# Optimization experiments

Hardware: AMD Instinct MI355X
Metric: run time of the kernel (lower is better)

Reference implementation:

```python
import jax, jax.numpy as jnp
import numpy as np

B, N, H = 8, 256, 128
IN_DIM = 2 * H + 3  # concat of row emb, col emb, 3-d edge embedding


def setup_inputs() -> dict:
    key = jax.random.key(0)
    ks = jax.random.split(key, 12)
    # xavier_uniform bound = sqrt(6/(fan_in+fan_out))
    def xavier(k, out_d, in_d, gain=1.0):
        bound = gain * np.sqrt(6.0 / (in_d + out_d))
        return jax.random.uniform(k, (out_d, in_d), jnp.float32, -bound, bound)
    return {
        "x_emb": jax.random.normal(ks[0], (B, N, H), jnp.float32),
        "pair_emb": jax.random.normal(ks[1], (B, N, N, H), jnp.float32),
        "pos": jax.random.normal(ks[2], (B, N, 3), jnp.float32),
        "coord_diff": jax.random.normal(ks[3], (B, N, N, 3), jnp.float32),
        "node_mask": jnp.ones((B, N, 1), jnp.float32),
        "pair_mask": jnp.ones((B, N, N, 1), jnp.float32),
        # dist_decoder: Linear(H, 3)
        "Wd": xavier(ks[4], 3, H),
        "bd": jnp.zeros((3,), jnp.float32),
        # coord_mlp: Linear(2H+3, H) -> SiLU -> Linear(H, H) -> SiLU -> Linear(H, 1, bias=False, gain=0.001)
        "W1": xavier(ks[5], H, IN_DIM),
        "b1": jnp.zeros((H,), jnp.float32),
        "W2": xavier(ks[6], H, H),
        "b2": jnp.zeros((H,), jnp.float32),
        "W3": xavier(ks[7], 1, H, gain=0.001),
    }


def reference(x_emb, pair_emb, pos, coord_diff, node_mask, pair_mask,
              Wd, bd, W1, b1, W2, b2, W3):
    # edge_emb: [B,N,N,3]
    edge_emb = jnp.einsum("bijh,dh->bijd", pair_emb, Wd) + bd
    # row/col broadcasts of node embeddings to pairwise shape [B,N,N,H]
    row = jnp.broadcast_to(x_emb[:, :, None, :], (B, N, N, H))
    col = jnp.broadcast_to(x_emb[:, None, :, :], (B, N, N, H))
    inp = jnp.concatenate([row, col, edge_emb], axis=-1)  # [B,N,N,2H+3]
    h = jax.nn.silu(jnp.einsum("bijk,hk->bijh", inp, W1) + b1)
    h = jax.nn.silu(jnp.einsum("bijh,gh->bijg", h, W2) + b2)
    s = jnp.einsum("bijh,oh->bijo", h, W3)  # [B,N,N,1]  (tanh=False path)
    trans = coord_diff * s * pair_mask  # [B,N,N,3]
    return pos + trans.sum(axis=2)
```

## Files before the change

kernel.cpp:

```cpp
#include <hip/hip_runtime.h>
#include <cstdint>
#include <cstddef>

#define B_ 8
#define N_ 256
#define H_ 128

typedef float f32x4 __attribute__((ext_vector_type(4)));
typedef int i32x4 __attribute__((ext_vector_type(4)));
typedef int i32x2 __attribute__((ext_vector_type(2)));
typedef __bf16 bf16x8 __attribute__((ext_vector_type(8)));
typedef unsigned int u32;
typedef unsigned short u16;

__device__ __forceinline__ u32 pack_bf16_pair(float lo, float hi) {
  u16 a = __builtin_bit_cast(u16, (__bf16)lo);
  u16 b = __builtin_bit_cast(u16, (__bf16)hi);
  return (u32)a | ((u32)b << 16);
}

__device__ __forceinline__ float silu_f(float x) {
  return x * __builtin_amdgcn_rcpf(1.0f + __expf(-x));
}

__device__ __forceinline__ f32x4 mfma16(i32x4 a, i32x4 b, f32x4 c) {
  return __builtin_amdgcn_mfma_f32_16x16x32_bf16(
      __builtin_bit_cast(bf16x8, a), __builtin_bit_cast(bf16x8, b), c, 0, 0, 0);
}

__global__ void prep_ru_kernel(const float* __restrict__ x_emb,
                               const float* __restrict__ W1,
                               const float* __restrict__ b1,
                               const float* __restrict__ bd,
                               float* __restrict__ R,
                               float* __restrict__ U) {
  __shared__ float xs[16][H_];
  const int t = threadIdx.x;
  const int row0 = blockIdx.x * 16;
#pragma unroll
  for (int r = 0; r < 16; ++r)
    xs[r][t] = x_emb[(size_t)(row0 + r) * H_ + t];
  __syncthreads();

  const float* w1g = W1 + (size_t)t * 259;
  float accR[16], accU[16];
#pragma unroll
  for (int r = 0; r < 16; ++r) { accR[r] = 0.f; accU[r] = 0.f; }
  for (int h = 0; h < H_; ++h) {
    float wa = w1g[h];
    float wb = w1g[128 + h];
#pragma unroll
    for (int r = 0; r < 16; ++r) {
      accR[r] += xs[r][h] * wa;
      accU[r] += xs[r][h] * wb;
    }
  }
  float bias = b1[t] + bd[0] * w1g[256] + bd[1] * w1g[257] + bd[2] * w1g[258];
#pragma unroll
  for (int r = 0; r < 16; ++r) {
    int n = (row0 + r) & (N_ - 1);
    R[(size_t)(row0 + r) * H_ + t] = accR[r];
    U[(size_t)(row0 + r) * H_ + (t ^ ((n & 7) << 2))] = accU[r] + bias;
  }
}

__global__ void prep_w_kernel(const float* __restrict__ W1,
                              const float* __restrict__ Wd,
                              const float* __restrict__ W2,
                              u16* __restrict__ We_b,
                              u16* __restrict__ W2_b) {
  const int idx = blockIdx.x * 256 + threadIdx.x;
  const int g = idx >> 7, h = idx & 127;
  const float* w1g = W1 + (size_t)g * 259 + 256;
  float we = w1g[0] * Wd[h] + w1g[1] * Wd[128 + h] + w1g[2] * Wd[256 + h];
  int se = (h >> 3) ^ (g & 7);
  We_b[g * 128 + (se << 3) + (h & 7)] = __builtin_bit_cast(u16, (__bf16)we);
  int s2 = (h >> 2) ^ (g & 7);
  W2_b[g * 128 + (s2 << 2) + (h & 3)] = __builtin_bit_cast(u16, (__bf16)W2[idx]);
}

__launch_bounds__(1024, 4)
__global__ void posupd_main(const float* __restrict__ pe,
                            const float* __restrict__ cd,
                            const float* __restrict__ pmask,
                            const float* __restrict__ b2,
                            const float* __restrict__ W3,
                            const float* __restrict__ R,
                            const float* __restrict__ U,
                            const uint4* __restrict__ Wcomb,
                            float* __restrict__ partial) {
  __shared__ uint4 ldsv[6144];
  char* lds = (char*)ldsv;
  const int tid = threadIdx.x;
  const int lane = tid & 63, wv = tid >> 6;
  const int bid = blockIdx.x;
  const int b = bid >> 8;
  const int rem = bid & 255;
  const int ig = rem >> 2, jg = rem & 3;

  const uint4* Usrc = (const uint4*)(U + ((size_t)b * N_ + jg * 64) * H_);
#pragma unroll
  for (int c = 0; c < 6; ++c) {
    int k = wv * 6 + c;
    const uint4* src = (k < 64) ? (Wcomb + (k << 6) + lane)
                                : (Usrc + ((k - 64) << 6) + lane);
    *reinterpret_cast<uint4*>(lds + (k << 10) + (lane << 4)) = *src;
  }
  __syncthreads();

  const int tok = lane & 15, kg = lane >> 4;
  const int iw = wv & 3, jtw = wv >> 2;
  const int i = ig * 4 + iw;
  const int jl = jtw * 16 + tok;
  const size_t bi = (size_t)b * N_ + i;
  const int jgl = jg * 64 + jl;

  const float* perow = pe + (bi * N_ + jgl) * H_;
  i32x4 bpe[4];
#pragma unroll
  for (int kt = 0; kt < 4; ++kt) {
    const float* p = perow + kt * 32 + kg * 8;
    f32x4 lo = *reinterpret_cast<const f32x4*>(p);
    f32x4 hi = *reinterpret_cast<const f32x4*>(p + 4);
    i32x4 f;
    f.x = (int)pack_bf16_pair(lo.x, lo.y);
    f.y = (int)pack_bf16_pair(lo.z, lo.w);
    f.z = (int)pack_bf16_pair(hi.x, hi.y);
    f.w = (int)pack_bf16_pair(hi.z, hi.w);
    bpe[kt] = f;
  }

  f32x4 a1[8];
#pragma unroll
  for (int mt = 0; mt < 8; ++mt) { a1[mt].x = a1[mt].y = a1[mt].z = a1[mt].w = 0.f; }
#pragma unroll
  for (int kt = 0; kt < 4; ++kt) {
#pragma unroll
    for (int mt = 0; mt < 8; ++mt) {
      int g = mt * 16 + tok;
      int off = (g << 8) + (((kt << 6) + (kg << 4)) ^ ((g & 7) << 4));
      i32x4 afr = *reinterpret_cast<const i32x4*>(lds + off);
      a1[mt] = mfma16(afr, bpe[kt], a1[mt]);
    }
  }

  const float* Rrow = R + bi * H_;
  u32 pk0[8], pk1[8];
#pragma unroll
  for (int mt = 0; mt < 8; ++mt) {
    int ch = mt * 16 + kg * 4;
    f32x4 rr = *reinterpret_cast<const f32x4*>(Rrow + ch);
    int ub = 65536 + (jl << 9) + ((ch << 2) ^ ((jl & 7) << 4));
    f32x4 uu = *reinterpret_cast<const f32x4*>(lds + ub);
    float h0 = silu_f(a1[mt].x + rr.x + uu.x);
    float h1 = silu_f(a1[mt].y + rr.y + uu.y);
    float h2 = silu_f(a1[mt].z + rr.z + uu.z);
    float h3 = silu_f(a1[mt].w + rr.w + uu.w);
    pk0[mt] = pack_bf16_pair(h0, h1);
    pk1[mt] = pack_bf16_pair(h2, h3);
  }

  f32x4 a2[8];
#pragma unroll
  for (int mt = 0; mt < 8; ++mt) { a2[mt].x = a2[mt].y = a2[mt].z = a2[mt].w = 0.f; }
#pragma unroll
  for (int kt2 = 0; kt2 < 4; ++kt2) {
    i32x4 bfr;
    bfr.x = (int)pk0[2 * kt2];
    bfr.y = (int)pk1[2 * kt2];
    bfr.z = (int)pk0[2 * kt2 + 1];
    bfr.w = (int)pk1[2 * kt2 + 1];
#pragma unroll
    for (int mt = 0; mt < 8; ++mt) {
      int g = mt * 16 + tok;
      int base = 32768 + (g << 8);
      int sw = (g & 7) << 3;
      i32x2 alo = *reinterpret_cast<const i32x2*>(lds + base + (((kt2 << 6) + (kg << 3)) ^ sw));
      i32x2 ahi = *reinterpret_cast<const i32x2*>(lds + base + (((kt2 << 6) + 32 + (kg << 3)) ^ sw));
      i32x4 afr;
      afr.x = alo.x; afr.y = alo.y; afr.z = ahi.x; afr.w = ahi.y;
      a2[mt] = mfma16(afr, bfr, a2[mt]);
    }
  }

  float sp = 0.f;
#pragma unroll
  for (int mt = 0; mt < 8; ++mt) {
    int ch = mt * 16 + kg * 4;
    f32x4 bb = *reinterpret_cast<const f32x4*>(b2 + ch);
    f32x4 ww = *reinterpret_cast<const f32x4*>(W3 + ch);
    sp += silu_f(a2[mt].x + bb.x) * ww.x;
    sp += silu_f(a2[mt].y + bb.y) * ww.y;
    sp += silu_f(a2[mt].z + bb.z) * ww.z;
    sp += silu_f(a2[mt].w + bb.w) * ww.w;
  }

  size_t pidx = bi * N_ + jgl;
  float sm = sp * pmask[pidx];
  const float* c3 = cd + pidx * 3;
  float aX = sm * c3[0], aY = sm * c3[1], aZ = sm * c3[2];
#pragma unroll
  for (int m = 1; m < 64; m <<= 1) {
    aX += __shfl_xor(aX, m);
    aY += __shfl_xor(aY, m);
    aZ += __shfl_xor(aZ, m);
  }
  if (lane == 0) {
    float* pp = partial + ((bi << 4) + (jg << 2) + jtw) * 3;
    pp[0] = aX; pp[1] = aY; pp[2] = aZ;
  }
}

__global__ void reduce_out(const float* __restrict__ partial,
                           const float* __restrict__ pos,
                           float* __restrict__ out) {
  int t = blockIdx.x * 256 + threadIdx.x;
  if (t >= B_ * N_) return;
  const float* p = partial + (size_t)t * 48;
  float s0 = 0.f, s1 = 0.f, s2 = 0.f;
#pragma unroll
  for (int q = 0; q < 16; ++q) {
    s0 += p[q * 3 + 0];
    s1 += p[q * 3 + 1];
    s2 += p[q * 3 + 2];
  }
  out[t * 3 + 0] = pos[t * 3 + 0] + s0;
  out[t * 3 + 1] = pos[t * 3 + 1] + s1;
  out[t * 3 + 2] = pos[t * 3 + 2] + s2;
}

extern "C" void kernel_launch(void* const* d_in, const int* in_sizes, int n_in,
                              void* d_out, int out_size, void* d_ws, size_t ws_size,
                              hipStream_t stream) {
  const float* x_emb      = (const float*)d_in[0];
  const float* pair_emb   = (const float*)d_in[1];
  const float* pos        = (const float*)d_in[2];
  const float* coord_diff = (const float*)d_in[3];
  const float* pair_mask  = (const float*)d_in[5];
  const float* Wd         = (const float*)d_in[6];
  const float* bd         = (const float*)d_in[7];
  const float* W1         = (const float*)d_in[8];
  const float* b1         = (const float*)d_in[9];
  const float* W2         = (const float*)d_in[10];
  const float* b2         = (const float*)d_in[11];
  const float* W3         = (const float*)d_in[12];
  float* out = (float*)d_out;

  char* ws = (char*)d_ws;
  float* R       = (float*)ws;
  float* U       = (float*)(ws + (1 << 20));
  u16*   WeB     = (u16*)(ws + (2 << 20));
  u16*   W2B     = (u16*)(ws + (2 << 20) + 32768);
  float* partial = (float*)(ws + (2 << 20) + 65536);

  hipLaunchKernelGGL(prep_ru_kernel, dim3((B_ * N_) / 16), dim3(128), 0, stream,
                     x_emb, W1, b1, bd, R, U);
  hipLaunchKernelGGL(prep_w_kernel, dim3(64), dim3(256), 0, stream,
                     W1, Wd, W2, WeB, W2B);
  hipLaunchKernelGGL(posupd_main, dim3(2048), dim3(1024), 0, stream,
                     pair_emb, coord_diff, pair_mask, b2, W3,
                     R, U, (const uint4*)(ws + (2 << 20)), partial);
  hipLaunchKernelGGL(reduce_out, dim3(8), dim3(256), 0, stream,
                     partial, pos, out);
}
```

Baseline: 462.4 us.

## Make main kernel persistent over j tiles with register-prefetched pair_emb and U

The main kernel now launches 512 blocks of 512 threads. Each block loads the combined weights into LDS once and then loops over 8 j-tiles of 32, prefetching the next tile's pair_emb rows and U slice into registers while the two MFMA stages run on the current tile. W2 is re-laid out so the second GEMM's A fragment becomes a single 16-byte LDS read instead of two 8-byte reads. Partial sums shrink to two per row, which simplifies the final reduce. The trade-offs are fewer blocks with more register pressure, and two extra barriers per iteration to refresh the U tile.

```diff
diff --git a/kernel.cpp b/kernel.cpp
--- a/kernel.cpp
+++ b/kernel.cpp
@@ -8,7 +8,6 @@
 
 typedef float f32x4 __attribute__((ext_vector_type(4)));
 typedef int i32x4 __attribute__((ext_vector_type(4)));
-typedef int i32x2 __attribute__((ext_vector_type(2)));
 typedef __bf16 bf16x8 __attribute__((ext_vector_type(8)));
 typedef unsigned int u32;
 typedef unsigned short u16;
@@ -75,11 +74,14 @@
   float we = w1g[0] * Wd[h] + w1g[1] * Wd[128 + h] + w1g[2] * Wd[256 + h];
   int se = (h >> 3) ^ (g & 7);
   We_b[g * 128 + (se << 3) + (h & 7)] = __builtin_bit_cast(u16, (__bf16)we);
-  int s2 = (h >> 2) ^ (g & 7);
-  W2_b[g * 128 + (s2 << 2) + (h & 3)] = __builtin_bit_cast(u16, (__bf16)W2[idx]);
-}
-
-__launch_bounds__(1024, 4)
+
+  int kt2 = h >> 5, m = (h >> 4) & 1, kg = (h >> 2) & 3, r = h & 3;
+  int gr = ((kt2 << 2) | kg) ^ (g & 7);
+  int e = (m << 2) | r;
+  W2_b[g * 128 + (gr << 3) + e] = __builtin_bit_cast(u16, (__bf16)W2[idx]);
+}
+
+__launch_bounds__(512, 4)
 __global__ void posupd_main(const float* __restrict__ pe,
                             const float* __restrict__ cd,
                             const float* __restrict__ pmask,
@@ -89,125 +91,163 @@
                             const float* __restrict__ U,
                             const uint4* __restrict__ Wcomb,
                             float* __restrict__ partial) {
-  __shared__ uint4 ldsv[6144];
+  __shared__ uint4 ldsv[5120];
   char* lds = (char*)ldsv;
   const int tid = threadIdx.x;
   const int lane = tid & 63, wv = tid >> 6;
-  const int bid = blockIdx.x;
-  const int b = bid >> 8;
-  const int rem = bid & 255;
-  const int ig = rem >> 2, jg = rem & 3;
-
-  const uint4* Usrc = (const uint4*)(U + ((size_t)b * N_ + jg * 64) * H_);
-#pragma unroll
-  for (int c = 0; c < 6; ++c) {
-    int k = wv * 6 + c;
-    const uint4* src = (k < 64) ? (Wcomb + (k << 6) + lane)
-                                : (Usrc + ((k - 64) << 6) + lane);
-    *reinterpret_cast<uint4*>(lds + (k << 10) + (lane << 4)) = *src;
-  }
-  __syncthreads();
-
-  const int tok = lane & 15, kg = lane >> 4;
+  const int b = blockIdx.x >> 6, ig = blockIdx.x & 63;
   const int iw = wv & 3, jtw = wv >> 2;
   const int i = ig * 4 + iw;
-  const int jl = jtw * 16 + tok;
+  const int tok = lane & 15, kg = lane >> 4;
+  const int jl = (jtw << 4) + tok;
   const size_t bi = (size_t)b * N_ + i;
-  const int jgl = jg * 64 + jl;
-
-  const float* perow = pe + (bi * N_ + jgl) * H_;
-  i32x4 bpe[4];
-#pragma unroll
-  for (int kt = 0; kt < 4; ++kt) {
-    const float* p = perow + kt * 32 + kg * 8;
-    f32x4 lo = *reinterpret_cast<const f32x4*>(p);
-    f32x4 hi = *reinterpret_cast<const f32x4*>(p + 4);
-    i32x4 f;
-    f.x = (int)pack_bf16_pair(lo.x, lo.y);
-    f.y = (int)pack_bf16_pair(lo.z, lo.w);
-    f.z = (int)pack_bf16_pair(hi.x, hi.y);
-    f.w = (int)pack_bf16_pair(hi.z, hi.w);
-    bpe[kt] = f;
-  }
-
-  f32x4 a1[8];
-#pragma unroll
-  for (int mt = 0; mt < 8; ++mt) { a1[mt].x = a1[mt].y = a1[mt].z = a1[mt].w = 0.f; }
-#pragma unroll
-  for (int kt = 0; kt < 4; ++kt) {
+
+  {
+    uint4 wb[8], ub[2];
+#pragma unroll
+    for (int c = 0; c < 8; ++c) wb[c] = Wcomb[(((wv << 3) + c) << 6) + lane];
+    const uint4* Us = (const uint4*)(U + (size_t)b * N_ * H_);
+#pragma unroll
+    for (int c = 0; c < 2; ++c) ub[c] = Us[(((wv << 1) + c) << 6) + lane];
+#pragma unroll
+    for (int c = 0; c < 8; ++c)
+      *reinterpret_cast<uint4*>(lds + (((wv << 3) + c) << 10) + (lane << 4)) = wb[c];
+#pragma unroll
+    for (int c = 0; c < 2; ++c)
+      *reinterpret_cast<uint4*>(lds + 65536 + (((wv << 1) + c) << 10) + (lane << 4)) = ub[c];
+  }
+
+  const float* peBase = pe + bi * N_ * H_;
+  const float* Rrow = R + bi * H_;
+  const int swz = (tok & 7) << 4;
+
+  f32x4 pf[8];
+  {
+    const float* p = peBase + (size_t)jl * H_;
+#pragma unroll
+    for (int kt = 0; kt < 4; ++kt) {
+      pf[2 * kt]     = *reinterpret_cast<const f32x4*>(p + kt * 32 + kg * 8);
+      pf[2 * kt + 1] = *reinterpret_cast<const f32x4*>(p + kt * 32 + kg * 8 + 4);
+    }
+  }
+  __syncthreads();
+
+  float accd0 = 0.f, accd1 = 0.f, accd2 = 0.f;
+
+  for (int jt = 0; jt < 8; ++jt) {
+    i32x4 bpe[4];
+#pragma unroll
+    for (int kt = 0; kt < 4; ++kt) {
+      f32x4 lo = pf[2 * kt], hi = pf[2 * kt + 1];
+      i32x4 f;
+      f.x = (int)pack_bf16_pair(lo.x, lo.y);
+      f.y = (int)pack_bf16_pair(lo.z, lo.w);
+      f.z = (int)pack_bf16_pair(hi.x, hi.y);
+      f.w = (int)pack_bf16_pair(hi.z, hi.w);
+      bpe[kt] = f;
+    }
+
+    uint4 ub0, ub1;
+    f32x4 pfn[8];
+    if (jt < 7) {
+      const uint4* Us = (const uint4*)(U + ((size_t)b * N_ + (jt + 1) * 32) * H_);
+      ub0 = Us[(((wv << 1) + 0) << 6) + lane];
+      ub1 = Us[(((wv << 1) + 1) << 6) + lane];
+      const float* p = peBase + (size_t)((jt + 1) * 32 + jl) * H_;
+#pragma unroll
+      for (int kt = 0; kt < 4; ++kt) {
+        pfn[2 * kt]     = *reinterpret_cast<const f32x4*>(p + kt * 32 + kg * 8);
+        pfn[2 * kt + 1] = *reinterpret_cast<const f32x4*>(p + kt * 32 + kg * 8 + 4);
+      }
+    }
+
+    f32x4 a1[8];
+#pragma unroll
+    for (int mt = 0; mt < 8; ++mt) { a1[mt].x = a1[mt].y = a1[mt].z = a1[mt].w = 0.f; }
+#pragma unroll
+    for (int kt = 0; kt < 4; ++kt) {
+#pragma unroll
+      for (int mt = 0; mt < 8; ++mt) {
+        int off = ((16 * mt + tok) << 8) + (((kt << 6) + (kg << 4)) ^ swz);
+        i32x4 afr = *reinterpret_cast<const i32x4*>(lds + off);
+        a1[mt] = mfma16(afr, bpe[kt], a1[mt]);
+      }
+    }
+
+    u32 pk0[8], pk1[8];
 #pragma unroll
     for (int mt = 0; mt < 8; ++mt) {
-      int g = mt * 16 + tok;
-      int off = (g << 8) + (((kt << 6) + (kg << 4)) ^ ((g & 7) << 4));
-      i32x4 afr = *reinterpret_cast<const i32x4*>(lds + off);
-      a1[mt] = mfma16(afr, bpe[kt], a1[mt]);
-    }
-  }
-
-  const float* Rrow = R + bi * H_;
-  u32 pk0[8], pk1[8];
-#pragma unroll
-  for (int mt = 0; mt < 8; ++mt) {
-    int ch = mt * 16 + kg * 4;
-    f32x4 rr = *reinterpret_cast<const f32x4*>(Rrow + ch);
-    int ub = 65536 + (jl << 9) + ((ch << 2) ^ ((jl & 7) << 4));
-    f32x4 uu = *reinterpret_cast<const f32x4*>(lds + ub);
-    float h0 = silu_f(a1[mt].x + rr.x + uu.x);
-    float h1 = silu_f(a1[mt].y + rr.y + uu.y);
-    float h2 = silu_f(a1[mt].z + rr.z + uu.z);
-    float h3 = silu_f(a1[mt].w + rr.w + uu.w);
-    pk0[mt] = pack_bf16_pair(h0, h1);
-    pk1[mt] = pack_bf16_pair(h2, h3);
-  }
-
-  f32x4 a2[8];
-#pragma unroll
-  for (int mt = 0; mt < 8; ++mt) { a2[mt].x = a2[mt].y = a2[mt].z = a2[mt].w = 0.f; }
-#pragma unroll
-  for (int kt2 = 0; kt2 < 4; ++kt2) {
-    i32x4 bfr;
-    bfr.x = (int)pk0[2 * kt2];
-    bfr.y = (int)pk1[2 * kt2];
-    bfr.z = (int)pk0[2 * kt2 + 1];
-    bfr.w = (int)pk1[2 * kt2 + 1];
+      int ch = mt * 16 + kg * 4;
+      f32x4 rr = *reinterpret_cast<const f32x4*>(Rrow + ch);
+      int ub = 65536 + (jl << 9) + ((ch << 2) ^ ((jl & 7) << 4));
+      f32x4 uu = *reinterpret_cast<const f32x4*>(lds + ub);
+      float h0 = silu_f(a1[mt].x + rr.x + uu.x);
+      float h1 = silu_f(a1[mt].y + rr.y + uu.y);
+      float h2 = silu_f(a1[mt].z + rr.z + uu.z);
+      float h3 = silu_f(a1[mt].w + rr.w + uu.w);
+      pk0[mt] = pack_bf16_pair(h0, h1);
+      pk1[mt] = pack_bf16_pair(h2, h3);
+    }
+
+    f32x4 a2[8];
+#pragma unroll
+    for (int mt = 0; mt < 8; ++mt) { a2[mt].x = a2[mt].y = a2[mt].z = a2[mt].w = 0.f; }
+#pragma unroll
+    for (int kt2 = 0; kt2 < 4; ++kt2) {
+      i32x4 bfr;
+      bfr.x = (int)pk0[2 * kt2];
+      bfr.y = (int)pk1[2 * kt2];
+      bfr.z = (int)pk0[2 * kt2 + 1];
+      bfr.w = (int)pk1[2 * kt2 + 1];
+#pragma unroll
+      for (int mt = 0; mt < 8; ++mt) {
+        int off = 32768 + ((16 * mt + tok) << 8) + (((kt2 << 6) + (kg << 4)) ^ swz);
+        i32x4 afr = *reinterpret_cast<const i32x4*>(lds + off);
+        a2[mt] = mfma16(afr, bfr, a2[mt]);
+      }
+    }
+
+    float sp = 0.f;
 #pragma unroll
     for (int mt = 0; mt < 8; ++mt) {
-      int g = mt * 16 + tok;
-      int base = 32768 + (g << 8);
-      int sw = (g & 7) << 3;
-      i32x2 alo = *reinterpret_cast<const i32x2*>(lds + base + (((kt2 << 6) + (kg << 3)) ^ sw));
-      i32x2 ahi = *reinterpret_cast<const i32x2*>(lds + base + (((kt2 << 6) + 32 + (kg << 3)) ^ sw));
-      i32x4 afr;
-      afr.x = alo.x; afr.y = alo.y; afr.z = ahi.x; afr.w = ahi.y;
-      a2[mt] = mfma16(afr, bfr, a2[mt]);
-    }
-  }
-
-  float sp = 0.f;
-#pragma unroll
-  for (int mt = 0; mt < 8; ++mt) {
-    int ch = mt * 16 + kg * 4;
-    f32x4 bb = *reinterpret_cast<const f32x4*>(b2 + ch);
-    f32x4 ww = *reinterpret_cast<const f32x4*>(W3 + ch);
-    sp += silu_f(a2[mt].x + bb.x) * ww.x;
-    sp += silu_f(a2[mt].y + bb.y) * ww.y;
-    sp += silu_f(a2[mt].z + bb.z) * ww.z;
-    sp += silu_f(a2[mt].w + bb.w) * ww.w;
-  }
-
-  size_t pidx = bi * N_ + jgl;
-  float sm = sp * pmask[pidx];
-  const float* c3 = cd + pidx * 3;
-  float aX = sm * c3[0], aY = sm * c3[1], aZ = sm * c3[2];
+      int ch = mt * 16 + kg * 4;
+      f32x4 bb = *reinterpret_cast<const f32x4*>(b2 + ch);
+      f32x4 ww = *reinterpret_cast<const f32x4*>(W3 + ch);
+      sp += silu_f(a2[mt].x + bb.x) * ww.x;
+      sp += silu_f(a2[mt].y + bb.y) * ww.y;
+      sp += silu_f(a2[mt].z + bb.z) * ww.z;
+      sp += silu_f(a2[mt].w + bb.w) * ww.w;
+    }
+
+    {
+      int j = (jt << 5) + jl;
+      size_t pidx = bi * N_ + j;
+      float sm = sp * pmask[pidx];
+      const float* c3 = cd + pidx * 3;
+      accd0 += sm * c3[0];
+      accd1 += sm * c3[1];
+      accd2 += sm * c3[2];
+    }
+
+    __syncthreads();
+    if (jt < 7) {
+      *reinterpret_cast<uint4*>(lds + 65536 + (((wv << 1) + 0) << 10) + (lane << 4)) = ub0;
+      *reinterpret_cast<uint4*>(lds + 65536 + (((wv << 1) + 1) << 10) + (lane << 4)) = ub1;
+      __syncthreads();
+#pragma unroll
+      for (int q = 0; q < 8; ++q) pf[q] = pfn[q];
+    }
+  }
+
 #pragma unroll
   for (int m = 1; m < 64; m <<= 1) {
-    aX += __shfl_xor(aX, m);
-    aY += __shfl_xor(aY, m);
-    aZ += __shfl_xor(aZ, m);
+    accd0 += __shfl_xor(accd0, m);
+    accd1 += __shfl_xor(accd1, m);
+    accd2 += __shfl_xor(accd2, m);
   }
   if (lane == 0) {
-    float* pp = partial + ((bi << 4) + (jg << 2) + jtw) * 3;
-    pp[0] = aX; pp[1] = aY; pp[2] = aZ;
+    float* pp = partial + ((bi << 1) + jtw) * 3;
+    pp[0] = accd0; pp[1] = accd1; pp[2] = accd2;
   }
 }
 
@@ -216,17 +256,10 @@
                            float* __restrict__ out) {
   int t = blockIdx.x * 256 + threadIdx.x;
   if (t >= B_ * N_) return;
-  const float* p = partial + (size_t)t * 48;
-  float s0 = 0.f, s1 = 0.f, s2 = 0.f;
-#pragma unroll
-  for (int q = 0; q < 16; ++q) {
-    s0 += p[q * 3 + 0];
-    s1 += p[q * 3 + 1];
-    s2 += p[q * 3 + 2];
-  }
-  out[t * 3 + 0] = pos[t * 3 + 0] + s0;
-  out[t * 3 + 1] = pos[t * 3 + 1] + s1;
-  out[t * 3 + 2] = pos[t * 3 + 2] + s2;
+  const float* p = partial + (size_t)t * 6;
+  out[t * 3 + 0] = pos[t * 3 + 0] + p[0] + p[3];
+  out[t * 3 + 1] = pos[t * 3 + 1] + p[1] + p[4];
+  out[t * 3 + 2] = pos[t * 3 + 2] + p[2] + p[5];
 }
 
 extern "C" void kernel_launch(void* const* d_in, const int* in_sizes, int n_in,
@@ -257,7 +290,7 @@
                      x_emb, W1, b1, bd, R, U);
   hipLaunchKernelGGL(prep_w_kernel, dim3(64), dim3(256), 0, stream,
                      W1, Wd, W2, WeB, W2B);
-  hipLaunchKernelGGL(posupd_main, dim3(2048), dim3(1024), 0, stream,
+  hipLaunchKernelGGL(posupd_main, dim3(512), dim3(512), 0, stream,
                      pair_emb, coord_diff, pair_mask, b2, W3,
                      R, U, (const uint4*)(ws + (2 << 20)), partial);
   hipLaunchKernelGGL(reduce_out, dim3(8), dim3(256), 0, stream,
```

Result: slower. 501.6 us (+8.5%).
